# Kernel optimization log

Hardware: AMD Instinct MI355X
Metric: run time of the kernel (lower is better)

## Reference

```python
import jax, jax.numpy as jnp
import numpy as np

B, NPTS = 2, 60000
NX, NY = 256, 256
PCR0, PCR1 = -32.0, -32.0
PS0, PS1 = 0.25, 0.25
MAXPP = 32      # max points per pillar
MAXP = 12000    # max pillars
C = 64          # lidar_channels
SENT = NX * NY  # sentinel pillar id (> any valid id)
NEG = -1e9
EPS = 1e-5


def setup_inputs():
    key = jax.random.key(0)
    ks = jax.random.split(key, 16)
    xy = jax.random.uniform(ks[0], (B, NPTS, 2), minval=-34.0, maxval=34.0)
    z = jax.random.uniform(ks[1], (B, NPTS, 1), minval=-3.0, maxval=1.0)
    ir = jax.random.uniform(ks[2], (B, NPTS, 2))
    pts = jnp.concatenate([xy, z, ir], axis=-1).astype(jnp.float32)
    mask = jax.random.uniform(ks[3], (B, NPTS)) < 0.98

    def lin(k, i, o):
        return (jax.random.normal(k, (i, o)) / np.sqrt(i)).astype(jnp.float32)

    inp = {"lidar_points": pts, "lidar_mask": mask,
           "w1": lin(ks[4], 10, 64), "b1": 0.01 * jax.random.normal(ks[5], (64,), jnp.float32),
           "g1": jnp.ones(64, jnp.float32), "be1": jnp.zeros(64, jnp.float32),
           "w2": lin(ks[6], 64, 64), "b2": 0.01 * jax.random.normal(ks[7], (64,), jnp.float32),
           "g2": jnp.ones(64, jnp.float32), "be2": jnp.zeros(64, jnp.float32)}
    for i, n in enumerate(["1", "2", "3"]):
        inp["cw" + n] = (jax.random.normal(ks[8 + i], (64, 64, 3, 3)) / np.sqrt(64 * 9)).astype(jnp.float32)
        inp["cb" + n] = 0.01 * jax.random.normal(ks[11 + i], (64,), jnp.float32)
        inp["cg" + n] = jnp.ones(64, jnp.float32)
        inp["cbe" + n] = jnp.zeros(64, jnp.float32)
    return inp


def bn1d(x, g, b):  # training-mode BN over rows (biased var), matches torch BatchNorm1d forward
    m = x.mean(0)
    v = ((x - m) ** 2).mean(0)
    return (x - m) * jax.lax.rsqrt(v + EPS) * g + b


def bn2d(x, g, b):  # training-mode BN over (N,H,W) per channel
    m = x.mean((0, 2, 3), keepdims=True)
    v = ((x - m) ** 2).mean((0, 2, 3), keepdims=True)
    return (x - m) * jax.lax.rsqrt(v + EPS) * g[None, :, None, None] + b[None, :, None, None]


def conv3(x, w, b):
    y = jax.lax.conv_general_dilated(x, w, (1, 1), 'SAME',
                                     dimension_numbers=('NCHW', 'OIHW', 'NCHW'))
    return y + b[None, :, None, None]


def pillarize(pts, msk):
    """pts: (N,5) xyzir, msk: (N,) bool -> padded pillar tensors (fixed shapes)."""
    n = pts.shape[0]
    ix = jnp.clip(((pts[:, 0] - PCR0) / PS0).astype(jnp.int32), 0, NX - 1)
    iy = jnp.clip(((pts[:, 1] - PCR1) / PS1).astype(jnp.int32), 0, NY - 1)
    pid = jnp.where(msk, iy * NX + ix, SENT)
    # sorted unique ids; keep the first (smallest) MAXP, like torch.unique + truncation
    spid = jnp.sort(pid)
    is_new = jnp.concatenate([jnp.array([True]), spid[1:] != spid[:-1]])
    urank = jnp.cumsum(is_new) - 1
    dest = jnp.where(is_new & (urank < MAXP) & (spid < SENT), urank, MAXP)
    uids = jnp.full((MAXP + 1,), SENT, dtype=pid.dtype).at[dest].set(spid)[:MAXP]  # ascending, SENT-padded
    inv = jnp.clip(jnp.searchsorted(uids, pid), 0, MAXP - 1)
    valid = (uids[inv] == pid) & (pid < SENT)
    # rank of each point within its pillar, in original point order (stable sort)
    seg = jnp.where(valid, inv, MAXP)
    order = jnp.argsort(seg)  # stable
    sseg = seg[order]
    pos = jnp.arange(n)
    first = jnp.concatenate([jnp.array([True]), sseg[1:] != sseg[:-1]])
    start = jax.lax.cummax(jnp.where(first, pos, 0))
    rank = jnp.zeros(n, jnp.int32).at[order].set((pos - start).astype(jnp.int32))
    keep = valid & (rank < MAXPP)  # first MAXPP points per pillar (matches truncation-then-mean)
    seg2 = jnp.where(keep, inv, MAXP)  # dump slot = MAXP
    cnt = jnp.zeros(MAXP + 1, pts.dtype).at[seg2].add(1.0)
    sums = jnp.zeros((MAXP + 1, 3), pts.dtype).at[seg2].add(jnp.where(keep[:, None], pts[:, :3], 0.0))
    mean = sums / jnp.maximum(cnt, 1.0)[:, None]
    ctr = mean[seg2]  # per-point pillar centroid (over kept points)
    gx = PCR0 + ((pid % NX).astype(pts.dtype) + 0.5) * PS0
    gy = PCR1 + ((pid // NX).astype(pts.dtype) + 0.5) * PS1
    aug = jnp.concatenate([pts, pts[:, :3] - ctr, gx[:, None], gy[:, None]], axis=1)  # (N,10)
    rk = jnp.minimum(rank, MAXPP - 1)
    pf = jnp.zeros((MAXP + 1, MAXPP, 10), pts.dtype).at[seg2, rk].set(
        jnp.where(keep[:, None], aug, 0.0))[:MAXP]
    pm = jnp.zeros((MAXP + 1, MAXPP), bool).at[seg2, rk].set(keep)[:MAXP]
    pvalid = uids < SENT
    coords = jnp.where(pvalid[:, None], jnp.stack([uids % NX, uids // NX], axis=-1), 0)
    return pf, pm, coords, pvalid


def pillar_net(pf, pm, w1, b1, g1, be1, w2, b2, g2, be2):
    npil, pp, ci = pf.shape
    x = pf.reshape(npil * pp, ci) @ w1 + b1
    x = jax.nn.relu(bn1d(x, g1, be1))
    x = x @ w2 + b2
    x = jax.nn.relu(bn1d(x, g2, be2))
    x = x.reshape(npil, pp, -1)
    x = jnp.where(pm[:, :, None], x, NEG)
    return x.max(axis=1)  # (npil, C)


def reference(lidar_points, lidar_mask, w1, b1, g1, be1, w2, b2, g2, be2,
              cw1, cb1, cg1, cbe1, cw2, cb2, cg2, cbe2, cw3, cb3, cg3, cbe3):
    pf, pm, coords, pvalid = jax.vmap(pillarize)(lidar_points, lidar_mask)
    # pillar net is applied per batch element in the original loop -> per-sample BN stats
    feat = jax.vmap(lambda a, m: pillar_net(a, m, w1, b1, g1, be1, w2, b2, g2, be2))(pf, pm)
    lin = coords[..., 1] * NX + coords[..., 0]          # (B, MAXP)
    f = jnp.where(pvalid[..., None], feat, 0.0)          # padded pillars contribute nothing
    bev = jax.vmap(lambda l, ff: jnp.zeros((NY * NX, C), ff.dtype).at[l].add(ff))(lin, f)
    bev = bev.reshape(-1, NY, NX, C).transpose(0, 3, 1, 2)  # (B,C,NY,NX)
    x = jax.nn.relu(bn2d(conv3(bev, cw1, cb1), cg1, cbe1))
    x = jax.nn.relu(bn2d(conv3(x, cw2, cb2), cg2, cbe2))
    x = jax.nn.relu(bn2d(conv3(x, cw3, cb3), cg3, cbe3))
    return x
```

## Files before the change

### kernel.cpp

```cpp
#include <hip/hip_runtime.h>

#define NPTS 60000
#define NXG 256
#define NCELL 65536
#define MAXP 12000
#define MAXPP 32
#define NROWS (MAXP*MAXPP)

typedef float f32x32 __attribute__((ext_vector_type(32)));
typedef float f32x4  __attribute__((ext_vector_type(4)));
typedef short s16x8  __attribute__((ext_vector_type(8)));

__device__ __forceinline__ short to_bf16(float f){
  unsigned u = __float_as_uint(f);
  unsigned r = (u + 0x7FFFu + ((u>>16)&1u)) >> 16;
  return (short)r;
}

__global__ void compute_pid(const float* __restrict__ pts, const void* __restrict__ maskp,
                            int* __restrict__ pid, int* __restrict__ pptr,
                            int* __restrict__ ccnt){
  __shared__ int cf32, cbig;
  if (threadIdx.x==0){ cf32=0; cbig=0; }
  __syncthreads();
  {
    int lf=0, lb=0;
    const unsigned* mu = (const unsigned*)maskp;
    for (int k=0;k<4;k++){
      unsigned x = mu[threadIdx.x*4+k];
      if (x==0x3f800000u) lf++;
      else if (x>1u) lb++;
    }
    if (lf) atomicAdd(&cf32, lf);
    if (lb) atomicAdd(&cbig, lb);
  }
  __syncthreads();
  int mode = (cf32>64) ? 2 : ((cbig>0) ? 1 : 0);
  int i = blockIdx.x*blockDim.x + threadIdx.x;
  if (i>=NPTS) return;
  int b = blockIdx.y;
  int gi = b*NPTS+i;
  bool m;
  if (mode==0)      m = ((const int*)maskp)[gi]!=0;
  else if (mode==1) m = ((const unsigned char*)maskp)[gi]!=0;
  else              m = ((const float*)maskp)[gi]!=0.f;
  int cell = -1;
  if (m){
    float x = pts[(size_t)gi*5+0], y = pts[(size_t)gi*5+1];
    int ix = (int)((x - (-32.0f)) / 0.25f);
    ix = ix<0?0:(ix>255?255:ix);
    int iy = (int)((y - (-32.0f)) / 0.25f);
    iy = iy<0?0:(iy>255?255:iy);
    cell = iy*NXG + ix;
    atomicAdd(&ccnt[b*NCELL+cell], 1);
  }
  pid[gi] = cell;
  pptr[gi] = -1;
}

__global__ __launch_bounds__(256) void scan_a(const int* __restrict__ ccnt,
                                              int2* __restrict__ bpart){
  int b = blockIdx.y, blk = blockIdx.x, t = threadIdx.x;
  int4 v = *(const int4*)&ccnt[b*NCELL + blk*1024 + t*4];
  int occ = (v.x>0)+(v.y>0)+(v.z>0)+(v.w>0);
  int cnt = v.x+v.y+v.z+v.w;
  #pragma unroll
  for (int off=32; off>0; off>>=1){
    occ += __shfl_xor(occ, off, 64);
    cnt += __shfl_xor(cnt, off, 64);
  }
  __shared__ int so[4], sc[4];
  int wv = t>>6, lane = t&63;
  if (lane==0){ so[wv]=occ; sc[wv]=cnt; }
  __syncthreads();
  if (t==0) bpart[b*64+blk] = make_int2(so[0]+so[1]+so[2]+so[3], sc[0]+sc[1]+sc[2]+sc[3]);
}

__global__ __launch_bounds__(256) void scan_b(const int* __restrict__ ccnt,
    const int2* __restrict__ bpart,
    int* __restrict__ crank, int* __restrict__ cstart, int* __restrict__ pcell,
    int* __restrict__ misc, int* __restrict__ heavy){
  __shared__ int swo[4], swc[4], sk[4];
  __shared__ int bo_, bc_;
  int b = blockIdx.y, blk = blockIdx.x, t = threadIdx.x;
  int wv = t>>6, lane = t&63;
  if (t < 64){
    int2 p = bpart[b*64+t];
    int po = (t<blk)? p.x : 0;
    int pc = (t<blk)? p.y : 0;
    int to = p.x;
    int tc = p.y;
    #pragma unroll
    for (int off=32; off>0; off>>=1){
      po += __shfl_xor(po, off, 64);
      pc += __shfl_xor(pc, off, 64);
      to += __shfl_xor(to, off, 64);
      tc += __shfl_xor(tc, off, 64);
    }
    if (t==0){
      bo_ = po; bc_ = pc;
      if (blk==0){
        misc[1+b] = (to < MAXP) ? to : MAXP;
        misc[5+b] = tc;
      }
    }
  }
  int4 v = *(const int4*)&ccnt[b*NCELL + blk*1024 + t*4];
  int occ = (v.x>0)+(v.y>0)+(v.z>0)+(v.w>0);
  int cnt = v.x+v.y+v.z+v.w;
  int io = occ, ic = cnt;
  #pragma unroll
  for (int off=1; off<64; off<<=1){
    int ao = __shfl_up(io, off, 64);
    int ac = __shfl_up(ic, off, 64);
    if (lane >= off){ io += ao; ic += ac; }
  }
  if (lane==63){ swo[wv]=io; swc[wv]=ic; }
  __syncthreads();
  int wvo=0, wvc=0;
  #pragma unroll
  for (int w2=0; w2<4; w2++){
    if (w2<wv){ wvo += swo[w2]; wvc += swc[w2]; }
  }
  int eo = bo_ + wvo + io - occ;
  int ec = bc_ + wvc + ic - cnt;
  int kept = 0;
  int cellb = blk*1024 + t*4;
  int vv[4] = {v.x,v.y,v.z,v.w};
  #pragma unroll
  for (int j=0;j<4;j++){
    int c = cellb+j; int val = vv[j];
    if (val>0){
      crank[b*NCELL+c]=eo; cstart[b*NCELL+c]=ec;
      if (eo<MAXP){
        pcell[b*MAXP+eo]=c;
        kept += (val<MAXPP)? val : MAXPP;
        if (val>MAXPP){
          int hi = atomicAdd(&heavy[b],1);
          if (hi<64) heavy[2 + b*64 + hi] = c;
        }
      }
      eo++; ec+=val;
    }
  }
  #pragma unroll
  for (int off=32; off>0; off>>=1) kept += __shfl_xor(kept, off, 64);
  if (lane==0) sk[wv]=kept;
  __syncthreads();
  if (t==0) atomicAdd(&misc[3+b], sk[0]+sk[1]+sk[2]+sk[3]);
}

__global__ void scatter_points(const int* __restrict__ pid, const int* __restrict__ ccnt,
    const int* __restrict__ crank, const int* __restrict__ cstart,
    int* __restrict__ ctmp, int* __restrict__ plist, int* __restrict__ pptr){
  int i = blockIdx.x*blockDim.x + threadIdx.x;
  if (i>=NPTS) return;
  int b = blockIdx.y;
  int gi = b*NPTS+i;
  int cell = pid[gi];
  if (cell<0) return;
  int bc = b*NCELL+cell;
  int pos = cstart[bc] + atomicAdd(&ctmp[bc],1);
  plist[b*NPTS+pos] = i;
  int r = crank[bc];
  if (r>=0 && r<MAXP && ccnt[bc]<=MAXPP) pptr[gi] = r;
}

__global__ void heavy_select(const int* __restrict__ ccnt, const int* __restrict__ crank,
    const int* __restrict__ cstart, const int* __restrict__ plist,
    const int* __restrict__ heavy, int* __restrict__ pptr){
  int b = blockIdx.y;
  int hn = heavy[b]; if (hn>64) hn=64;
  if ((int)blockIdx.x >= hn) return;
  int cell = heavy[2 + b*64 + blockIdx.x];
  int bc = b*NCELL+cell;
  int cnt = ccnt[bc], start = cstart[bc], pr = crank[bc];
  for (int e=threadIdx.x; e<cnt; e+=blockDim.x){
    int pe = plist[b*NPTS+start+e];
    int rank=0;
    for (int k=0;k<cnt;k++) rank += (plist[b*NPTS+start+k] < pe);
    if (rank<MAXPP) pptr[b*NPTS+pe] = pr;
  }
}

__global__ __launch_bounds__(256) void gather_cpts(const float* __restrict__ pts,
    const int* __restrict__ pid, const int* __restrict__ pptr,
    const int* __restrict__ plist, const int* __restrict__ misc,
    float* __restrict__ cpts, float* __restrict__ psum){
  int pos = blockIdx.x*256 + threadIdx.x;
  int b = blockIdx.y;
  if (pos >= misc[5+b]) return;
  int i = plist[b*NPTS+pos];
  int gi = b*NPTS+i;
  const float* qp = &pts[(size_t)gi*5];
  float x=qp[0], y=qp[1], z=qp[2], i1=qp[3], i2=qp[4];
  int cell = pid[gi];
  int rid = pptr[gi];
  float gx = -32.0f + ((float)(cell&255)+0.5f)*0.25f;
  float gy = -32.0f + ((float)(cell>>8)+0.5f)*0.25f;
  float4* cp = (float4*)&cpts[(size_t)(b*NPTS+pos)*8];
  cp[0] = make_float4(x,y,z,i1);
  cp[1] = make_float4(i2,gx,gy,__int_as_float(rid));
  if (rid>=0){
    float* s = &psum[(size_t)(b*MAXP+rid)*4];
    atomicAdd(s+0,x); atomicAdd(s+1,y); atomicAdd(s+2,z); atomicAdd(s+3,1.f);
  }
}

__global__ void centroid_fin(float* __restrict__ psum){
  int i = blockIdx.x*blockDim.x + threadIdx.x;
  if (i>=2*MAXP) return;
  float* s = &psum[(size_t)i*4];
  float inv = 1.0f / fmaxf(s[3],1.0f);
  s[0]*=inv; s[1]*=inv; s[2]*=inv;
}

#define MM_ACC(K,V) { if ((K)<32) m0[(K)&31]+=(V); else if ((K)<64) m1[((K)-32)&31]+=(V); else m2+=(V); }
__global__ __launch_bounds__(256) void moments(const float* __restrict__ cpts,
    const float* __restrict__ psum, const int* __restrict__ misc,
    float* __restrict__ lstat){
  int b = blockIdx.y;
  int n = misc[5+b];
  f32x32 m0, m1; float m2 = 0.f;
  #pragma unroll
  for (int j=0;j<32;j++){ m0[j]=0.f; m1[j]=0.f; }
  for (int pos = blockIdx.x*256+threadIdx.x; pos<n; pos += gridDim.x*256){
    const float4* cp = (const float4*)&cpts[(size_t)(b*NPTS+pos)*8];
    float4 f1 = cp[0], f2 = cp[1];
    int rid = __float_as_int(f2.w);
    if (rid<0) continue;
    float4 mc = *(const float4*)&psum[(size_t)(b*MAXP+rid)*4];
    float aug[10] = {f1.x,f1.y,f1.z,f1.w,f2.x,
                     f1.x-mc.x, f1.y-mc.y, f1.z-mc.z, f2.y, f2.z};
    #pragma unroll
    for (int d=0; d<10; d++){
      #pragma unroll
      for (int e=d; e<10; e++){
        const int k = d*10 - d*(d-1)/2 + (e-d);
        MM_ACC(k, aug[d]*aug[e]);
      }
      const int kl = 55+d;
      MM_ACC(kl, aug[d]);
    }
  }
  int lane = threadIdx.x & 63;
  int rep = ((blockIdx.x*256+threadIdx.x)>>6) & 15;
  float* dst = &lstat[(size_t)(rep*2+b)*65];
  #pragma unroll
  for (int j=0;j<32;j++){
    float v = m0[j];
    #pragma unroll
    for (int off=32; off>0; off>>=1) v += __shfl_xor(v, off, 64);
    if (lane==0) atomicAdd(&dst[j], v);
  }
  #pragma unroll
  for (int j=0;j<32;j++){
    float v = m1[j];
    #pragma unroll
    for (int off=32; off>0; off>>=1) v += __shfl_xor(v, off, 64);
    if (lane==0) atomicAdd(&dst[32+j], v);
  }
  {
    float v = m2;
    #pragma unroll
    for (int off=32; off>0; off>>=1) v += __shfl_xor(v, off, 64);
    if (lane==0) atomicAdd(&dst[64], v);
  }
}

__global__ void stats_fin1(const float* __restrict__ w1, const float* __restrict__ b1,
    const float* __restrict__ g1, const float* __restrict__ be1,
    const float* __restrict__ w2, const float* __restrict__ b2,
    const float* __restrict__ lstat, float* __restrict__ stats,
    const int* __restrict__ misc){
  __shared__ float M[65];
  __shared__ float z0s[64];
  int b = blockIdx.x, c = threadIdx.x;
  for (int e=c; e<65; e+=64){
    float s=0.f;
    for (int r=0;r<16;r++) s += lstat[(size_t)(r*2+b)*65+e];
    M[e]=s;
  }
  __syncthreads();
  float* S = &stats[(size_t)b*512];
  float wcol[10];
  #pragma unroll
  for (int d=0;d<10;d++) wcol[d] = w1[d*64+c];
  float b1c = b1[c];
  float nk = (float)misc[3+b];
  const float N = (float)NROWS;
  float pad = N - nk;
  float lw = 0.f;
  #pragma unroll
  for (int d=0;d<10;d++) lw += M[55+d]*wcol[d];
  float s = nk*b1c + lw;
  float qq = nk*b1c*b1c + 2.f*b1c*lw;
  #pragma unroll
  for (int d=0; d<10; d++){
    #pragma unroll
    for (int e=d; e<10; e++){
      float m = M[d*10 - d*(d-1)/2 + (e-d)];
      qq += ((d==e)?1.f:2.f)*m*wcol[d]*wcol[e];
    }
  }
  float St = s + pad*b1c;
  float Qt = qq + pad*b1c*b1c;
  float mu = St/N;
  float var = fmaxf(Qt/N - mu*mu, 0.f);
  float sc = g1[c]*rsqrtf(var+1e-5f);
  float sh = be1[c]-mu*sc;
  S[256+c]=sc; S[320+c]=sh;
  float z0 = fmaxf(b1c*sc+sh, 0.f);
  z0s[c]=z0;
  __syncthreads();
  float t0 = b2[c];
  for (int i2=0;i2<64;i2++) t0 += z0s[i2]*w2[(size_t)i2*64+c];
  S[128+c]=pad*t0; S[192+c]=pad*t0*t0;
}

__global__ __launch_bounds__(256) void pillar_mlp(const float* __restrict__ cpts,
    const int* __restrict__ pcell, const int* __restrict__ cstart,
    const int* __restrict__ ccnt, const float* __restrict__ psum,
    const int* __restrict__ misc,
    const float* __restrict__ w1, const float* __restrict__ b1,
    const float* __restrict__ w2, const float* __restrict__ b2,
    const float* __restrict__ stats, float* __restrict__ l2stat,
    float* __restrict__ fmx, float* __restrict__ fmn){
  const int lane = threadIdx.x & 63;
  float w1c[10];
  #pragma unroll
  for (int d=0;d<10;d++) w1c[d] = w1[d*64+lane];
  f32x32 w2lo, w2hi;
  #pragma unroll
  for (int c=0;c<32;c++) w2lo[c] = w2[(size_t)c*64+lane];
  #pragma unroll
  for (int c=0;c<32;c++) w2hi[c] = w2[(size_t)(c+32)*64+lane];
  const float b1c = b1[lane], b2c = b2[lane];
  const float sc1_0 = stats[256+lane], sh1_0 = stats[320+lane];
  const float sc1_1 = stats[512+256+lane], sh1_1 = stats[512+320+lane];
  const int npil0 = misc[1], npil1 = misc[2];
  float s2_0=0.f, q2_0=0.f, s2_1=0.f, q2_1=0.f;

  const int wglobal = (blockIdx.x*256 + threadIdx.x) >> 6;
  const int nwaves = (gridDim.x*256) >> 6;
  for (int qq = wglobal; qq < 2*MAXP; qq += nwaves){
    int b = (qq >= MAXP) ? 1 : 0;
    int p = qq - b*MAXP;
    int npil = b ? npil1 : npil0;
    if (p >= npil) continue;
    int cell = pcell[b*MAXP+p];
    int bc = b*NCELL+cell;
    int cnt = ccnt[bc], start = cstart[bc];
    const float* mc = &psum[(size_t)(b*MAXP+p)*4];
    float mx = mc[0], my = mc[1], mz = mc[2];
    float gx = -32.0f + ((float)(cell&255)+0.5f)*0.25f;
    float gy = -32.0f + ((float)(cell>>8)+0.5f)*0.25f;
    float sc1 = b ? sc1_1 : sc1_0;
    float sh1 = b ? sh1_1 : sh1_0;
    float tmax = -1e30f, tmin = 1e30f;
    float s2 = 0.f, q2 = 0.f;
    for (int k=0; k<cnt; k++){
      const float4* cp = (const float4*)&cpts[(size_t)(b*NPTS+start+k)*8];
      float4 f1 = cp[0], f2 = cp[1];
      int rid = __float_as_int(f2.w);
      if (rid != p) continue;
      float x=f1.x, y=f1.y, z=f1.z, i1=f1.w, i2=f2.x;
      float acc = b1c;
      acc = fmaf(x, w1c[0], acc);
      acc = fmaf(y, w1c[1], acc);
      acc = fmaf(z, w1c[2], acc);
      acc = fmaf(i1, w1c[3], acc);
      acc = fmaf(i2, w1c[4], acc);
      acc = fmaf(x-mx, w1c[5], acc);
      acc = fmaf(y-my, w1c[6], acc);
      acc = fmaf(z-mz, w1c[7], acc);
      acc = fmaf(gx, w1c[8], acc);
      acc = fmaf(gy, w1c[9], acc);
      float zz = fmaxf(acc*sc1+sh1, 0.f);
      float t = b2c;
      #pragma unroll
      for (int c=0;c<32;c++){
        float zc = __int_as_float(__builtin_amdgcn_readlane(__float_as_int(zz), c));
        t = fmaf(zc, w2lo[c], t);
      }
      #pragma unroll
      for (int c=0;c<32;c++){
        float zc = __int_as_float(__builtin_amdgcn_readlane(__float_as_int(zz), c+32));
        t = fmaf(zc, w2hi[c], t);
      }
      tmax = fmaxf(tmax, t);
      tmin = fminf(tmin, t);
      s2 += t; q2 += t*t;
    }
    fmx[(size_t)(b*MAXP+p)*64 + lane] = tmax;
    fmn[(size_t)(b*MAXP+p)*64 + lane] = tmin;
    if (b){ s2_1 += s2; q2_1 += q2; } else { s2_0 += s2; q2_0 += q2; }
  }
  int rep = wglobal & 15;
  atomicAdd(&l2stat[((rep*2+0)*2+0)*64+lane], s2_0);
  atomicAdd(&l2stat[((rep*2+0)*2+1)*64+lane], q2_0);
  atomicAdd(&l2stat[((rep*2+1)*2+0)*64+lane], s2_1);
  atomicAdd(&l2stat[((rep*2+1)*2+1)*64+lane], q2_1);
}

__global__ void stats_fin2(const float* __restrict__ g2,const float* __restrict__ be2,
                           const float* __restrict__ l2stat, float* __restrict__ stats){
  int b = blockIdx.x, c = threadIdx.x;
  float* S = &stats[(size_t)b*512];
  float s = S[128+c], q = S[192+c];
  for (int r=0;r<16;r++){
    s += l2stat[((r*2+b)*2+0)*64+c];
    q += l2stat[((r*2+b)*2+1)*64+c];
  }
  const float N = (float)NROWS;
  float m = s/N;
  float v = fmaxf(q/N - m*m, 0.f);
  float sc = g2[c]*rsqrtf(v+1e-5f);
  S[384+c]=sc; S[448+c]=be2[c]-m*sc;
}

__global__ void scatter_bev(const float* __restrict__ fmx, const float* __restrict__ fmn,
                            const int* __restrict__ pcell, const int* __restrict__ misc,
                            const float* __restrict__ stats, short* __restrict__ bevh){
  int tid = blockIdx.x*256+threadIdx.x;
  if (tid >= 2*64*MAXP) return;
  int c = tid & 63;
  int bp = tid >> 6;
  int b = bp / MAXP;
  int p = bp - b*MAXP;
  if (p >= misc[1+b]) return;
  float sc2 = stats[(size_t)b*512+384+c], sh2 = stats[(size_t)b*512+448+c];
  float t = (sc2 >= 0.f) ? fmx[tid] : fmn[tid];
  float v = fmaxf(sc2*t+sh2, 0.f);
  int cell = pcell[b*MAXP+p];
  bevh[((size_t)((b<<16) + cell))*64 + c] = to_bf16(v);
}

__global__ void wcvt3(const float* __restrict__ w0, const float* __restrict__ w1,
                      const float* __restrict__ w2, short* __restrict__ wh){
  int t = blockIdx.x*256 + threadIdx.x;
  if (t >= 3*36864) return;
  int l = t / 36864, r = t - l*36864;
  const float* w = (l==0)? w0 : ((l==1)? w1 : w2);
  int ic = r & 63, oc = (r>>6)&63, tap = r>>12;
  wh[t] = to_bf16(w[(oc*64+ic)*9 + tap]);
}

#define MFMA16(A,B,C) __builtin_amdgcn_mfma_f32_16x16x32_bf16(A,B,C,0,0,0)

__global__ __launch_bounds__(256,2) void conv_mfma(const short* __restrict__ xh,
    const short* __restrict__ wh, const float* __restrict__ bias,
    const float* __restrict__ pstat, const float* __restrict__ pg, const float* __restrict__ pbe,
    short* __restrict__ outh, float* __restrict__ outf,
    float* __restrict__ stat){
  __shared__ short sX[18*18*40];
  __shared__ float sBN[128];
  __shared__ float ss[64], sq[64];
  const int tX = blockIdx.x*16, tY = blockIdx.y*16, b = blockIdx.z;
  const int t = threadIdx.x;
  const int lane = t & 63, wv = t >> 6;
  const int colx = lane & 15;
  const int kb = (lane >> 4) * 8;
  if (t < 64){
    ss[t]=0.f; sq[t]=0.f;
    if (pstat){
      const float n = 131072.f;
      float m = pstat[t]/n;
      float v = fmaxf(pstat[64+t]/n - m*m, 0.f);
      float sc = pg[t]*rsqrtf(v+1e-5f);
      sBN[t]=sc; sBN[64+t]=pbe[t]-m*sc;
    }
  }

  f32x4 a00={0.f,0.f,0.f,0.f}, a01=a00, a02=a00, a03=a00;
  f32x4 a10=a00, a11=a00, a12=a00, a13=a00;
  f32x4 a20=a00, a21=a00, a22=a00, a23=a00;
  f32x4 a30=a00, a31=a00, a32=a00, a33=a00;

  for (int h=0; h<2; ++h){
    __syncthreads();
    for (int e=t; e<1296; e+=256){
      int px = e>>2, j = e&3;
      int yy = px/18, xx = px - yy*18;
      int gy = tY+yy-1, gx = tX+xx-1;
      uint4 v = make_uint4(0,0,0,0);
      if ((unsigned)gy<256u && (unsigned)gx<256u){
        v = *(const uint4*)&xh[((size_t)((b<<16) + (gy<<8) + gx))*64 + h*32 + j*8];
        if (pstat){
          unsigned arr[4] = {v.x, v.y, v.z, v.w};
          #pragma unroll
          for (int j2=0;j2<4;j2++){
            unsigned wrd = arr[j2];
            int ch = h*32 + j*8 + j2*2;
            float lo = __uint_as_float(wrd<<16);
            float hi = __uint_as_float(wrd & 0xffff0000u);
            lo = fmaxf(lo*sBN[ch]+sBN[64+ch], 0.f);
            hi = fmaxf(hi*sBN[ch+1]+sBN[64+ch+1], 0.f);
            arr[j2] = (unsigned)(unsigned short)to_bf16(lo) |
                      (((unsigned)(unsigned short)to_bf16(hi))<<16);
          }
          v = make_uint4(arr[0],arr[1],arr[2],arr[3]);
        }
      }
      *(uint4*)&sX[px*40 + j*8] = v;
    }
    __syncthreads();
    #pragma unroll
    for (int tap=0; tap<9; ++tap){
      const int dy = tap/3, dx = tap - dy*3;
      const short* wb = wh + tap*4096 + colx*64 + h*32 + kb;
      s16x8 wA = *(const s16x8*)(wb);
      s16x8 wB = *(const s16x8*)(wb + 1024);
      s16x8 wC = *(const s16x8*)(wb + 2048);
      s16x8 wD = *(const s16x8*)(wb + 3072);
      s16x8 x0 = *(const s16x8*)&sX[((wv*4+0+dy)*18 + colx+dx)*40 + kb];
      s16x8 x1 = *(const s16x8*)&sX[((wv*4+1+dy)*18 + colx+dx)*40 + kb];
      s16x8 x2 = *(const s16x8*)&sX[((wv*4+2+dy)*18 + colx+dx)*40 + kb];
      s16x8 x3 = *(const s16x8*)&sX[((wv*4+3+dy)*18 + colx+dx)*40 + kb];
      a00 = MFMA16(wA,x0,a00); a01 = MFMA16(wA,x1,a01);
      a02 = MFMA16(wA,x2,a02); a03 = MFMA16(wA,x3,a03);
      a10 = MFMA16(wB,x0,a10); a11 = MFMA16(wB,x1,a11);
      a12 = MFMA16(wB,x2,a12); a13 = MFMA16(wB,x3,a13);
      a20 = MFMA16(wC,x0,a20); a21 = MFMA16(wC,x1,a21);
      a22 = MFMA16(wC,x2,a22); a23 = MFMA16(wC,x3,a23);
      a30 = MFMA16(wD,x0,a30); a31 = MFMA16(wD,x1,a31);
      a32 = MFMA16(wD,x2,a32); a33 = MFMA16(wD,x3,a33);
    }
  }
  const int ocl = (lane>>4)*4;
  #define DOG(G, A0,A1,A2,A3) { \
    const int oc0g = G*16 + ocl; \
    float bj0=bias[oc0g], bj1=bias[oc0g+1], bj2=bias[oc0g+2], bj3=bias[oc0g+3]; \
    float v00=A0[0]+bj0, v01=A0[1]+bj1, v02=A0[2]+bj2, v03=A0[3]+bj3; \
    float v10=A1[0]+bj0, v11=A1[1]+bj1, v12=A1[2]+bj2, v13=A1[3]+bj3; \
    float v20=A2[0]+bj0, v21=A2[1]+bj1, v22=A2[2]+bj2, v23=A2[3]+bj3; \
    float v30=A3[0]+bj0, v31=A3[1]+bj1, v32=A3[2]+bj2, v33=A3[3]+bj3; \
    float s0=v00+v10+v20+v30, q0=v00*v00+v10*v10+v20*v20+v30*v30; \
    float s1=v01+v11+v21+v31, q1=v01*v01+v11*v11+v21*v21+v31*v31; \
    float s2=v02+v12+v22+v32, q2=v02*v02+v12*v12+v22*v22+v32*v32; \
    float s3=v03+v13+v23+v33, q3=v03*v03+v13*v13+v23*v23+v33*v33; \
    s0+=__shfl_xor(s0,1,64); s0+=__shfl_xor(s0,2,64); s0+=__shfl_xor(s0,4,64); s0+=__shfl_xor(s0,8,64); \
    q0+=__shfl_xor(q0,1,64); q0+=__shfl_xor(q0,2,64); q0+=__shfl_xor(q0,4,64); q0+=__shfl_xor(q0,8,64); \
    s1+=__shfl_xor(s1,1,64); s1+=__shfl_xor(s1,2,64); s1+=__shfl_xor(s1,4,64); s1+=__shfl_xor(s1,8,64); \
    q1+=__shfl_xor(q1,1,64); q1+=__shfl_xor(q1,2,64); q1+=__shfl_xor(q1,4,64); q1+=__shfl_xor(q1,8,64); \
    s2+=__shfl_xor(s2,1,64); s2+=__shfl_xor(s2,2,64); s2+=__shfl_xor(s2,4,64); s2+=__shfl_xor(s2,8,64); \
    q2+=__shfl_xor(q2,1,64); q2+=__shfl_xor(q2,2,64); q2+=__shfl_xor(q2,4,64); q2+=__shfl_xor(q2,8,64); \
    s3+=__shfl_xor(s3,1,64); s3+=__shfl_xor(s3,2,64); s3+=__shfl_xor(s3,4,64); s3+=__shfl_xor(s3,8,64); \
    q3+=__shfl_xor(q3,1,64); q3+=__shfl_xor(q3,2,64); q3+=__shfl_xor(q3,4,64); q3+=__shfl_xor(q3,8,64); \
    if (colx==0){ \
      atomicAdd(&ss[oc0g],s0);   atomicAdd(&sq[oc0g],q0); \
      atomicAdd(&ss[oc0g+1],s1); atomicAdd(&sq[oc0g+1],q1); \
      atomicAdd(&ss[oc0g+2],s2); atomicAdd(&sq[oc0g+2],q2); \
      atomicAdd(&ss[oc0g+3],s3); atomicAdd(&sq[oc0g+3],q3); \
    } \
    if (outh){ \
      size_t pb = (size_t)((b<<16) + tX + colx); \
      *(short4*)&outh[(pb + ((tY+wv*4+0)<<8))*64 + oc0g] = make_short4(to_bf16(v00),to_bf16(v01),to_bf16(v02),to_bf16(v03)); \
      *(short4*)&outh[(pb + ((tY+wv*4+1)<<8))*64 + oc0g] = make_short4(to_bf16(v10),to_bf16(v11),to_bf16(v12),to_bf16(v13)); \
      *(short4*)&outh[(pb + ((tY+wv*4+2)<<8))*64 + oc0g] = make_short4(to_bf16(v20),to_bf16(v21),to_bf16(v22),to_bf16(v23)); \
      *(short4*)&outh[(pb + ((tY+wv*4+3)<<8))*64 + oc0g] = make_short4(to_bf16(v30),to_bf16(v31),to_bf16(v32),to_bf16(v33)); \
    } else { \
      size_t cb0 = (((size_t)(b*64+oc0g))<<16) + ((tY+wv*4)<<8) + tX + colx; \
      outf[cb0          ] = v00; outf[cb0+(1<<16)      ] = v01; outf[cb0+(2<<16)      ] = v02; outf[cb0+(3<<16)      ] = v03; \
      outf[cb0+256      ] = v10; outf[cb0+(1<<16)+256  ] = v11; outf[cb0+(2<<16)+256  ] = v12; outf[cb0+(3<<16)+256  ] = v13; \
      outf[cb0+512      ] = v20; outf[cb0+(1<<16)+512  ] = v21; outf[cb0+(2<<16)+512  ] = v22; outf[cb0+(3<<16)+512  ] = v23; \
      outf[cb0+768      ] = v30; outf[cb0+(1<<16)+768  ] = v31; outf[cb0+(2<<16)+768  ] = v32; outf[cb0+(3<<16)+768  ] = v33; \
    } \
  }
  DOG(0, a00,a01,a02,a03)
  DOG(1, a10,a11,a12,a13)
  DOG(2, a20,a21,a22,a23)
  DOG(3, a30,a31,a32,a33)
  #undef DOG
  __syncthreads();
  if (t < 64){
    atomicAdd(&stat[t],    ss[t]);
    atomicAdd(&stat[64+t], sq[t]);
  }
}

__global__ void bn_fin(float* __restrict__ bnst, const float* __restrict__ g, const float* __restrict__ be){
  int c = threadIdx.x;
  const float n = 131072.f;
  float m = bnst[c]/n;
  float v = fmaxf(bnst[64+c]/n - m*m, 0.f);
  float sc = g[c]*rsqrtf(v+1e-5f);
  bnst[128+c]=sc; bnst[192+c]=be[c]-m*sc;
}

__global__ __launch_bounds__(256) void bn_apply(float* __restrict__ x, const float* __restrict__ bnst){
  size_t idx = (size_t)blockIdx.x*256 + threadIdx.x;
  size_t stride = (size_t)gridDim.x*256;
  float4* p = (float4*)x;
  for (size_t k=idx; k<2097152ULL; k+=stride){
    int c = (int)((k>>14)&63);
    float sc = bnst[128+c], sh = bnst[192+c];
    float4 v = p[k];
    v.x=fmaxf(v.x*sc+sh,0.f); v.y=fmaxf(v.y*sc+sh,0.f);
    v.z=fmaxf(v.z*sc+sh,0.f); v.w=fmaxf(v.w*sc+sh,0.f);
    p[k]=v;
  }
}

extern "C" void kernel_launch(void* const* d_in, const int* in_sizes, int n_in,
                              void* d_out, int out_size, void* d_ws, size_t ws_size,
                              hipStream_t stream){
  const float* pts  = (const float*)d_in[0];
  const void*  mask = d_in[1];
  const float* w1 = (const float*)d_in[2];
  const float* b1 = (const float*)d_in[3];
  const float* g1 = (const float*)d_in[4];
  const float* be1= (const float*)d_in[5];
  const float* w2 = (const float*)d_in[6];
  const float* b2 = (const float*)d_in[7];
  const float* g2 = (const float*)d_in[8];
  const float* be2= (const float*)d_in[9];
  const float* cw[3]  = {(const float*)d_in[10],(const float*)d_in[14],(const float*)d_in[18]};
  const float* cb[3]  = {(const float*)d_in[11],(const float*)d_in[15],(const float*)d_in[19]};
  const float* cg[3]  = {(const float*)d_in[12],(const float*)d_in[16],(const float*)d_in[20]};
  const float* cbe[3] = {(const float*)d_in[13],(const float*)d_in[17],(const float*)d_in[21]};
  float* out = (float*)d_out;

  char* W = (char*)d_ws;
  size_t off = 0;
  auto A = [&](size_t n){ size_t r = off; off = (off + n + 255) & ~(size_t)255; return r; };
  short*    BIGH  = (short*)   (W + A((size_t)2*NCELL*64*2));
  short*    OUT1H = (short*)   (W + A((size_t)2*NCELL*64*2));
  int*      PID   = (int*)     (W + A((size_t)2*NPTS*4));
  int*      CRANK = (int*)     (W + A((size_t)2*NCELL*4));
  int*      CSTART= (int*)     (W + A((size_t)2*NCELL*4));
  int*      PLIST = (int*)     (W + A((size_t)2*NPTS*4));
  int*      PPTR  = (int*)     (W + A((size_t)2*NPTS*4));
  int*      PCELL = (int*)     (W + A((size_t)2*MAXP*4));
  float*    CPTS  = (float*)   (W + A((size_t)2*NPTS*8*4));
  float*    FMX   = (float*)   (W + A((size_t)2*MAXP*64*4));
  float*    FMN   = (float*)   (W + A((size_t)2*MAXP*64*4));
  short*    WH    = (short*)   (W + A((size_t)3*36864*2));
  int2*     BPART = (int2*)    (W + A((size_t)2*64*8));
  size_t zbeg = off;
  int*      CCNT  = (int*)     (W + A((size_t)2*NCELL*4));
  int*      CTMP  = (int*)     (W + A((size_t)2*NCELL*4));
  float*    PSUM  = (float*)   (W + A((size_t)2*MAXP*16));
  float*    STATS = (float*)   (W + A((size_t)2*512*4));
  float*    LSTAT = (float*)   (W + A((size_t)16*2*65*4));
  float*    L2STAT= (float*)   (W + A((size_t)16*2*2*64*4));
  float*    BNST  = (float*)   (W + A((size_t)3*256*4));
  int*      HEAVY = (int*)     (W + A((size_t)(2+2*64)*4));
  int*      MISC  = (int*)     (W + A(256));
  size_t zend = off;

  hipMemsetAsync(BIGH, 0, (size_t)2*NCELL*64*2, stream);
  hipMemsetAsync(W+zbeg, 0, zend-zbeg, stream);

  dim3 perPt((NPTS+255)/256, 2);

  compute_pid<<<perPt,256,0,stream>>>(pts, mask, PID, PPTR, CCNT);
  wcvt3<<<432,256,0,stream>>>(cw[0], cw[1], cw[2], WH);
  scan_a<<<dim3(64,2),256,0,stream>>>(CCNT, BPART);
  scan_b<<<dim3(64,2),256,0,stream>>>(CCNT, BPART, CRANK, CSTART, PCELL, MISC, HEAVY);
  scatter_points<<<perPt,256,0,stream>>>(PID, CCNT, CRANK, CSTART, CTMP, PLIST, PPTR);
  heavy_select<<<dim3(64,2),64,0,stream>>>(CCNT, CRANK, CSTART, PLIST, HEAVY, PPTR);
  gather_cpts<<<perPt,256,0,stream>>>(pts, PID, PPTR, PLIST, MISC, CPTS, PSUM);
  centroid_fin<<<(2*MAXP+255)/256,256,0,stream>>>(PSUM);
  moments<<<dim3(120,2),256,0,stream>>>(CPTS, PSUM, MISC, LSTAT);
  stats_fin1<<<2,64,0,stream>>>(w1, b1, g1, be1, w2, b2, LSTAT, STATS, MISC);
  pillar_mlp<<<2048,256,0,stream>>>(CPTS, PCELL, CSTART, CCNT, PSUM, MISC,
                                    w1, b1, w2, b2, STATS, L2STAT, FMX, FMN);
  stats_fin2<<<2,64,0,stream>>>(g2, be2, L2STAT, STATS);
  scatter_bev<<<(2*64*MAXP+255)/256,256,0,stream>>>(FMX, FMN, PCELL, MISC, STATS, BIGH);

  conv_mfma<<<dim3(16,16,2),256,0,stream>>>(BIGH, WH, cb[0], nullptr, nullptr, nullptr,
                                            OUT1H, nullptr, BNST);
  conv_mfma<<<dim3(16,16,2),256,0,stream>>>(OUT1H, WH+36864, cb[1], BNST, cg[0], cbe[0],
                                            BIGH, nullptr, BNST+256);
  conv_mfma<<<dim3(16,16,2),256,0,stream>>>(BIGH, WH+2*36864, cb[2], BNST+256, cg[1], cbe[1],
                                            nullptr, out, BNST+512);
  bn_fin<<<1,64,0,stream>>>(BNST+512, cg[2], cbe[2]);
  bn_apply<<<2048,256,0,stream>>>(out, BNST+512);
}
```

Baseline: 262.4 us.

## Split conv output channels across blocks and stage weights in LDS

After: 242.8 us. -7.5%, faster.

```diff
diff --git a/kernel.cpp b/kernel.cpp
--- a/kernel.cpp
+++ b/kernel.cpp
@@ -448,34 +448,32 @@
 
 #define MFMA16(A,B,C) __builtin_amdgcn_mfma_f32_16x16x32_bf16(A,B,C,0,0,0)
 
-__global__ __launch_bounds__(256,2) void conv_mfma(const short* __restrict__ xh,
+__global__ __launch_bounds__(256,3) void conv_mfma(const short* __restrict__ xh,
     const short* __restrict__ wh, const float* __restrict__ bias,
     const float* __restrict__ pstat, const float* __restrict__ pg, const float* __restrict__ pbe,
     short* __restrict__ outh, float* __restrict__ outf,
     float* __restrict__ stat){
   __shared__ short sX[18*18*40];
+  __shared__ short sW[288*40];
   __shared__ float sBN[128];
-  __shared__ float ss[64], sq[64];
-  const int tX = blockIdx.x*16, tY = blockIdx.y*16, b = blockIdx.z;
+  __shared__ float ss[32], sq[32];
+  const int tX = blockIdx.x*16, tY = blockIdx.y*16;
+  const int b = blockIdx.z >> 1, ocbase = (blockIdx.z & 1)*32;
   const int t = threadIdx.x;
   const int lane = t & 63, wv = t >> 6;
   const int colx = lane & 15;
   const int kb = (lane >> 4) * 8;
-  if (t < 64){
-    ss[t]=0.f; sq[t]=0.f;
-    if (pstat){
-      const float n = 131072.f;
-      float m = pstat[t]/n;
-      float v = fmaxf(pstat[64+t]/n - m*m, 0.f);
-      float sc = pg[t]*rsqrtf(v+1e-5f);
-      sBN[t]=sc; sBN[64+t]=pbe[t]-m*sc;
-    }
+  if (t < 32){ ss[t]=0.f; sq[t]=0.f; }
+  if (t < 64 && pstat){
+    const float n = 131072.f;
+    float m = pstat[t]/n;
+    float v = fmaxf(pstat[64+t]/n - m*m, 0.f);
+    float sc = pg[t]*rsqrtf(v+1e-5f);
+    sBN[t]=sc; sBN[64+t]=pbe[t]-m*sc;
   }
 
   f32x4 a00={0.f,0.f,0.f,0.f}, a01=a00, a02=a00, a03=a00;
   f32x4 a10=a00, a11=a00, a12=a00, a13=a00;
-  f32x4 a20=a00, a21=a00, a22=a00, a23=a00;
-  f32x4 a30=a00, a31=a00, a32=a00, a33=a00;
 
   for (int h=0; h<2; ++h){
     __syncthreads();
@@ -504,15 +502,18 @@
       }
       *(uint4*)&sX[px*40 + j*8] = v;
     }
+    for (int e=t; e<1152; e+=256){
+      int row = e>>2, j = e&3;
+      int tap = row>>5, ocl = row&31;
+      uint4 v = *(const uint4*)&wh[(size_t)tap*4096 + (ocbase+ocl)*64 + h*32 + j*8];
+      *(uint4*)&sW[row*40 + j*8] = v;
+    }
     __syncthreads();
     #pragma unroll
     for (int tap=0; tap<9; ++tap){
       const int dy = tap/3, dx = tap - dy*3;
-      const short* wb = wh + tap*4096 + colx*64 + h*32 + kb;
-      s16x8 wA = *(const s16x8*)(wb);
-      s16x8 wB = *(const s16x8*)(wb + 1024);
-      s16x8 wC = *(const s16x8*)(wb + 2048);
-      s16x8 wD = *(const s16x8*)(wb + 3072);
+      s16x8 wA = *(const s16x8*)&sW[(tap*32 +  0 + colx)*40 + kb];
+      s16x8 wB = *(const s16x8*)&sW[(tap*32 + 16 + colx)*40 + kb];
       s16x8 x0 = *(const s16x8*)&sX[((wv*4+0+dy)*18 + colx+dx)*40 + kb];
       s16x8 x1 = *(const s16x8*)&sX[((wv*4+1+dy)*18 + colx+dx)*40 + kb];
       s16x8 x2 = *(const s16x8*)&sX[((wv*4+2+dy)*18 + colx+dx)*40 + kb];
@@ -521,15 +522,12 @@
       a02 = MFMA16(wA,x2,a02); a03 = MFMA16(wA,x3,a03);
       a10 = MFMA16(wB,x0,a10); a11 = MFMA16(wB,x1,a11);
       a12 = MFMA16(wB,x2,a12); a13 = MFMA16(wB,x3,a13);
-      a20 = MFMA16(wC,x0,a20); a21 = MFMA16(wC,x1,a21);
-      a22 = MFMA16(wC,x2,a22); a23 = MFMA16(wC,x3,a23);
-      a30 = MFMA16(wD,x0,a30); a31 = MFMA16(wD,x1,a31);
-      a32 = MFMA16(wD,x2,a32); a33 = MFMA16(wD,x3,a33);
     }
   }
   const int ocl = (lane>>4)*4;
   #define DOG(G, A0,A1,A2,A3) { \
-    const int oc0g = G*16 + ocl; \
+    const int lc = G*16 + ocl; \
+    const int oc0g = ocbase + lc; \
     float bj0=bias[oc0g], bj1=bias[oc0g+1], bj2=bias[oc0g+2], bj3=bias[oc0g+3]; \
     float v00=A0[0]+bj0, v01=A0[1]+bj1, v02=A0[2]+bj2, v03=A0[3]+bj3; \
     float v10=A1[0]+bj0, v11=A1[1]+bj1, v12=A1[2]+bj2, v13=A1[3]+bj3; \
@@ -548,10 +546,10 @@
     s3+=__shfl_xor(s3,1,64); s3+=__shfl_xor(s3,2,64); s3+=__shfl_xor(s3,4,64); s3+=__shfl_xor(s3,8,64); \
     q3+=__shfl_xor(q3,1,64); q3+=__shfl_xor(q3,2,64); q3+=__shfl_xor(q3,4,64); q3+=__shfl_xor(q3,8,64); \
     if (colx==0){ \
-      atomicAdd(&ss[oc0g],s0);   atomicAdd(&sq[oc0g],q0); \
-      atomicAdd(&ss[oc0g+1],s1); atomicAdd(&sq[oc0g+1],q1); \
-      atomicAdd(&ss[oc0g+2],s2); atomicAdd(&sq[oc0g+2],q2); \
-      atomicAdd(&ss[oc0g+3],s3); atomicAdd(&sq[oc0g+3],q3); \
+      atomicAdd(&ss[lc],s0);   atomicAdd(&sq[lc],q0); \
+      atomicAdd(&ss[lc+1],s1); atomicAdd(&sq[lc+1],q1); \
+      atomicAdd(&ss[lc+2],s2); atomicAdd(&sq[lc+2],q2); \
+      atomicAdd(&ss[lc+3],s3); atomicAdd(&sq[lc+3],q3); \
     } \
     if (outh){ \
       size_t pb = (size_t)((b<<16) + tX + colx); \
@@ -569,13 +567,11 @@
   }
   DOG(0, a00,a01,a02,a03)
   DOG(1, a10,a11,a12,a13)
-  DOG(2, a20,a21,a22,a23)
-  DOG(3, a30,a31,a32,a33)
   #undef DOG
   __syncthreads();
-  if (t < 64){
-    atomicAdd(&stat[t],    ss[t]);
-    atomicAdd(&stat[64+t], sq[t]);
+  if (t < 32){
+    atomicAdd(&stat[ocbase+t],    ss[t]);
+    atomicAdd(&stat[64+ocbase+t], sq[t]);
   }
 }
 
@@ -669,11 +665,11 @@
   stats_fin2<<<2,64,0,stream>>>(g2, be2, L2STAT, STATS);
   scatter_bev<<<(2*64*MAXP+255)/256,256,0,stream>>>(FMX, FMN, PCELL, MISC, STATS, BIGH);
 
-  conv_mfma<<<dim3(16,16,2),256,0,stream>>>(BIGH, WH, cb[0], nullptr, nullptr, nullptr,
+  conv_mfma<<<dim3(16,16,4),256,0,stream>>>(BIGH, WH, cb[0], nullptr, nullptr, nullptr,
                                             OUT1H, nullptr, BNST);
-  conv_mfma<<<dim3(16,16,2),256,0,stream>>>(OUT1H, WH+36864, cb[1], BNST, cg[0], cbe[0],
+  conv_mfma<<<dim3(16,16,4),256,0,stream>>>(OUT1H, WH+36864, cb[1], BNST, cg[0], cbe[0],
                                             BIGH, nullptr, BNST+256);
-  conv_mfma<<<dim3(16,16,2),256,0,stream>>>(BIGH, WH+2*36864, cb[2], BNST+256, cg[1], cbe[1],
+  conv_mfma<<<dim3(16,16,4),256,0,stream>>>(BIGH, WH+2*36864, cb[2], BNST+256, cg[1], cbe[1],
                                             nullptr, out, BNST+512);
   bn_fin<<<1,64,0,stream>>>(BNST+512, cg[2], cbe[2]);
   bn_apply<<<2048,256,0,stream>>>(out, BNST+512);
```
